# Optimization experiments

Hardware: AMD Instinct MI355X
Metric: run time of the kernel (lower is better)

## Reference

```python
import jax, jax.numpy as jnp
import numpy as np

N = 8192
IN_F = 128
OUT_F = 128
ALPHA = 0.2  # LeakyReLU negative slope
NEG_INF = -9e15


def setup_inputs() -> dict:
    key = jax.random.key(0)
    k1, k2, k3, k4, k5 = jax.random.split(key, 5)
    mole_out = jax.random.normal(k1, (N, IN_F), dtype=jnp.float32)
    adj = jax.random.randint(k2, (N, N), 0, 2, dtype=jnp.int32)
    # nn.Linear(in_features, out_features, bias=False): y = x @ W  (W stored as [in, out])
    W = jax.random.normal(k3, (IN_F, OUT_F), dtype=jnp.float32) / np.sqrt(IN_F)
    # nn.Linear(2*out_features, 1, bias=False) weight split into a1 (for Wh_i) and a2 (for Wh_j)
    a1 = jax.random.normal(k4, (OUT_F,), dtype=jnp.float32) / np.sqrt(2 * OUT_F)
    a2 = jax.random.normal(k5, (OUT_F,), dtype=jnp.float32) / np.sqrt(2 * OUT_F)
    return {"mole_out": mole_out, "adj": adj, "W": W, "a1": a1, "a2": a2}


def reference(mole_out, adj, W, a1, a2):
    Wh = mole_out @ W                       # (N, F)
    # a([Wh_i || Wh_j]) = a1.Wh_i + a2.Wh_j  -- avoids the O(N^2*2F) concat tensor
    s1 = Wh @ a1                            # (N,)
    s2 = Wh @ a2                            # (N,)
    e = jax.nn.leaky_relu(s1[:, None] + s2[None, :], negative_slope=ALPHA)  # (N, N)
    att = jnp.where(adj > 0, e, NEG_INF)
    att = jax.nn.softmax(att, axis=1)       # row softmax over neighbors j
    # dropout_gnn = 0.0 -> identity
    h_prime = att @ Wh                      # (N, F)
    return jax.nn.elu(h_prime)              # concat=True branch
```

## Files before the change

### kernel.cpp

```cpp
#include <hip/hip_runtime.h>
#include <hip/hip_bf16.h>

#define NROW 8192
#define NF   128
#define LOG2E 1.4426950408889634f

typedef float f32x4  __attribute__((ext_vector_type(4)));
typedef int   i32x4  __attribute__((ext_vector_type(4)));
typedef short bf16x8 __attribute__((ext_vector_type(8)));
typedef short bf16x4 __attribute__((ext_vector_type(4)));
typedef unsigned long long u64;

__device__ __forceinline__ short f2bf(float f) {
    union { float f; unsigned u; } v; v.f = f;
    unsigned r = v.u + 0x7FFFu + ((v.u >> 16) & 1u);
    return (short)(r >> 16);
}

__device__ __forceinline__ void gload_lds16(const short* g, short* l) {
    __builtin_amdgcn_global_load_lds(
        (const __attribute__((address_space(1))) void*)g,
        (__attribute__((address_space(3))) void*)l, 16, 0, 0);
}


__global__ __launch_bounds__(256) void k0_wt(const float* __restrict__ W,
                                             short* __restrict__ WT) {
    int idx = blockIdx.x * 256 + threadIdx.x;
    int c = idx >> 7, k = idx & 127;
    WT[c * NF + k] = f2bf(W[k * NF + c]);
}

__global__ __launch_bounds__(256) void k1_wh(const float* __restrict__ mo,
        const short* __restrict__ WT,
        const float* __restrict__ a1, const float* __restrict__ a2,
        short* __restrict__ WhT, float* __restrict__ s1g, float* __restrict__ s2g) {
    __shared__ float s_lds[2][32];
    int t = threadIdx.x;
    int w = t >> 6, l = t & 63, lg = l >> 4, lr = l & 15;
    int rows0 = blockIdx.x * 32;
    if (t < 64) s_lds[t >> 5][t & 31] = 0.0f;
    __syncthreads();

    f32x4 acc[2][2] = {};
#pragma unroll
    for (int ks = 0; ks < 4; ++ks) {
        bf16x8 a[2], b[2];
#pragma unroll
        for (int rt = 0; rt < 2; ++rt) {
            const float* ap = mo + (size_t)(rows0 + rt*16 + lr) * NF + ks*32 + lg*8;
            f32x4 x0 = *(const f32x4*)ap;
            f32x4 x1 = *(const f32x4*)(ap + 4);
#pragma unroll
            for (int e = 0; e < 4; ++e) { a[rt][e] = f2bf(x0[e]); a[rt][4+e] = f2bf(x1[e]); }
        }
#pragma unroll
        for (int ct = 0; ct < 2; ++ct) {
            int c = w*32 + ct*16 + lr;
            b[ct] = *(const bf16x8*)(WT + c*NF + ks*32 + lg*8);
        }
#pragma unroll
        for (int rt = 0; rt < 2; ++rt)
#pragma unroll
            for (int ct = 0; ct < 2; ++ct)
                acc[rt][ct] = __builtin_amdgcn_mfma_f32_16x16x32_bf16(a[rt], b[ct], acc[rt][ct], 0, 0, 0);
    }

#pragma unroll
    for (int rt = 0; rt < 2; ++rt) {
        float p1[4] = {0,0,0,0}, p2[4] = {0,0,0,0};
#pragma unroll
        for (int ct = 0; ct < 2; ++ct) {
            int c = w*32 + ct*16 + lr;
            float a1c = a1[c], a2c = a2[c];
            bf16x4 wv;
#pragma unroll
            for (int g = 0; g < 4; ++g) {
                float v = acc[rt][ct][g];
                wv[g] = f2bf(v);
                p1[g] += v * a1c;
                p2[g] += v * a2c;
            }
            int r0 = rows0 + rt*16 + lg*4;
            size_t off = (size_t)(r0 >> 6) * 8192 + (size_t)(c >> 4) * 1024
                       + (size_t)((r0 >> 5) & 1) * 512 + (size_t)((r0 >> 3) & 3) * 128
                       + (size_t)(c & 15) * 8 + (size_t)(r0 & 7);
            *(bf16x4*)(WhT + off) = wv;
        }
#pragma unroll
        for (int off = 1; off < 16; off <<= 1) {
#pragma unroll
            for (int g = 0; g < 4; ++g) {
                p1[g] += __shfl_xor(p1[g], off);
                p2[g] += __shfl_xor(p2[g], off);
            }
        }
        if (lr == 0) {
            int rloc = rt*16 + lg*4;
#pragma unroll
            for (int g = 0; g < 4; ++g) {
                atomicAdd(&s_lds[0][rloc+g], p1[g]);
                atomicAdd(&s_lds[1][rloc+g], p2[g]);
            }
        }
    }
    __syncthreads();
    if (t < 32)       s1g[rows0 + t]        = s_lds[0][t] * LOG2E;
    else if (t < 64)  s2g[rows0 + (t - 32)] = s_lds[1][t - 32] * LOG2E;
}

__global__ __launch_bounds__(256, 4) void k2_main(
        const int* __restrict__ adj, const short* __restrict__ WhT,
        const float* __restrict__ s1g, const float* __restrict__ s2g,
        float* __restrict__ numP, float* __restrict__ zP,
        int S, int npb) {
    __shared__ __attribute__((aligned(16))) short Bl[2][8192];
    __shared__ __attribute__((aligned(16))) float s2l[1024];

    int t = threadIdx.x, w = t >> 6, l = t & 63;
    int lo = l & 15, hi = l >> 4;
    int b = blockIdx.x, jseg = b % S, rg = b / S;
    int wrows0 = (rg << 6) + (w << 4);
    int j0 = jseg * npb;
    int NT = npb >> 6;

    for (int i = t; i < (npb >> 2); i += 256)
        ((f32x4*)s2l)[i] = ((const f32x4*)(s2g + j0))[i];

    float s1v = s1g[wrows0 + lo];
    const int* arow = adj + (size_t)wrows0 * NROW + j0 + l;

    f32x4 acc[8] = {};
    float z = 0.0f;

    int An[16];
#pragma unroll
    for (int r = 0; r < 16; ++r)
        An[r] = __builtin_nontemporal_load(arow + r * NROW);
    {
        const short* gs = WhT + (size_t)(j0 >> 6) * 8192 + w*2048 + l*8;
        short* ds = &Bl[0][w*2048];
#pragma unroll
        for (int r4 = 0; r4 < 4; ++r4)
            gload_lds16(gs + r4*512, ds + r4*512);
    }
    __syncthreads();

    int cur = 0;
    for (int it = 0; it < NT; ++it) {
        int more = (it + 1 < NT);
        if (more) {
            const short* gs = WhT + (size_t)((j0 + ((it+1) << 6)) >> 6) * 8192 + w*2048 + l*8;
            short* ds = &Bl[cur ^ 1][w*2048];
#pragma unroll
            for (int r4 = 0; r4 < 4; ++r4)
                gload_lds16(gs + r4*512, ds + r4*512);
        }
        u64 bmq = 0;
#pragma unroll
        for (int r = 0; r < 16; ++r) {
            u64 br = __ballot(An[r] > 0);
            if (more) An[r] = __builtin_nontemporal_load(arow + r * NROW + ((it + 1) << 6));
            bmq = (lo == r) ? br : bmq;
        }
#pragma unroll
        for (int ks = 0; ks < 2; ++ks) {
            unsigned bits = (unsigned)(bmq >> ((ks << 5) + hi * 8)) & 0xffu;
            int js = (it << 6) + ks * 32 + hi * 8;
            f32x4 sa = *(const f32x4*)(s2l + js);
            f32x4 sb = *(const f32x4*)(s2l + js + 4);
            float p[8];
#pragma unroll
            for (int e = 0; e < 4; ++e) {
                float x, pe;
                x = s1v + sa[e]; pe = exp2f(fmaxf(x, 0.2f * x));
                p[e]     = ((bits >> e) & 1) ? pe : 0.0f;        z += p[e];
                x = s1v + sb[e]; pe = exp2f(fmaxf(x, 0.2f * x));
                p[4 + e] = ((bits >> (4 + e)) & 1) ? pe : 0.0f;  z += p[4 + e];
            }
            union { bf16x8 v8; __hip_bfloat162 h2[4]; } fau;
#pragma unroll
            for (int q = 0; q < 4; ++q)
                fau.h2[q] = __float22bfloat162_rn(make_float2(p[2*q], p[2*q + 1]));
            const short* Bc = &Bl[cur][ks * 512 + l * 8];
#pragma unroll
            for (int ct = 0; ct < 8; ++ct) {
                bf16x8 bv = *(const bf16x8*)(Bc + ct * 1024);
                acc[ct] = __builtin_amdgcn_mfma_f32_16x16x32_bf16(fau.v8, bv, acc[ct], 0, 0, 0);
            }
        }
        asm volatile("s_waitcnt vmcnt(16)" ::: "memory");
        __builtin_amdgcn_sched_barrier(0);
        __builtin_amdgcn_s_barrier();
        __builtin_amdgcn_sched_barrier(0);
        cur ^= 1;
    }

    z += __shfl_xor(z, 16);
    z += __shfl_xor(z, 32);
    if (l < 16) zP[(size_t)jseg * NROW + wrows0 + lo] = z;

    size_t obase = (size_t)jseg * NROW * NF;
#pragma unroll
    for (int ct = 0; ct < 8; ++ct) {
        int cc = ct * 16 + lo;
        int r0 = wrows0 + hi * 4;
#pragma unroll
        for (int g = 0; g < 4; ++g)
            numP[obase + (size_t)(r0 + g) * NF + cc] = acc[ct][g];
    }
}

__global__ __launch_bounds__(256) void k3_reduce(const float* __restrict__ numP,
        const float* __restrict__ zP, float* __restrict__ out, int S) {
    int idx = (blockIdx.x * 256 + threadIdx.x) * 4;
    int r = idx >> 7;
    f32x4 num = {};
    float zz = 0.0f;
    for (int s = 0; s < S; ++s) {
        f32x4 v = *(const f32x4*)(numP + (size_t)s * (NROW * NF) + idx);
        num += v;
        zz  += zP[s * NROW + r];
    }
    f32x4 o;
#pragma unroll
    for (int e = 0; e < 4; ++e) {
        float h = num[e] / zz;
        o[e] = (h > 0.0f) ? h : expm1f(h);
    }
    *(f32x4*)(out + idx) = o;
}

extern "C" void kernel_launch(void* const* d_in, const int* in_sizes, int n_in,
                              void* d_out, int out_size, void* d_ws, size_t ws_size,
                              hipStream_t stream) {
    const float* mo  = (const float*)d_in[0];
    const int*   adj = (const int*)d_in[1];
    const float* W   = (const float*)d_in[2];
    const float* a1  = (const float*)d_in[3];
    const float* a2  = (const float*)d_in[4];
    float* out = (float*)d_out;

    char* p = (char*)d_ws;
    short* WT  = (short*)p;  p += (size_t)NF * NF * 2;
    short* WhT = (short*)p;  p += (size_t)NF * NROW * 2;
    float* s1  = (float*)p;  p += (size_t)NROW * 4;
    float* s2  = (float*)p;  p += (size_t)NROW * 4;
    float* zP  = (float*)p;  p += (size_t)8 * NROW * 4;
    size_t fixed = (size_t)(p - (char*)d_ws);

    int S = 8;
    while (S > 1 && fixed + (size_t)S * NROW * NF * 4 > ws_size) S >>= 1;
    float* numP = (float*)p;
    if (fixed + (size_t)S * NROW * NF * 4 > ws_size) numP = out;

    k0_wt<<<dim3(64), dim3(256), 0, stream>>>(W, WT);
    k1_wh<<<dim3(256), dim3(256), 0, stream>>>(mo, WT, a1, a2, WhT, s1, s2);
    k2_main<<<dim3((NROW / 64) * S), dim3(256), 0, stream>>>(adj, WhT, s1, s2, numP, zP, S, NROW / S);
    k3_reduce<<<dim3(NROW * NF / 1024), dim3(256), 0, stream>>>(numP, zP, out, S);
}
```

Measured before the change: 97.03 us.

## Precompute adjacency bitmask in fused pre-kernel and stage it into LDS

Adjacency ballot-to-bitmask conversion moves out of the main attention kernel into extra blocks fused into the Wh projection kernel, which write a packed u64 bitmask to workspace. The main kernel loads its bitmask slice into LDS up front, so its loop no longer streams the 256MB int32 adjacency. The WhT tile drops from double to single buffering with full barriers, which frees LDS for the mask but serializes load and compute. The S-shrinking workspace fallback is removed.

```diff
diff --git a/kernel.cpp b/kernel.cpp
--- a/kernel.cpp
+++ b/kernel.cpp
@@ -4,6 +4,7 @@
 #define NROW 8192
 #define NF   128
 #define LOG2E 1.4426950408889634f
+#define NBM  ((NROW / 64) * (NROW / 512))
 
 typedef float f32x4  __attribute__((ext_vector_type(4)));
 typedef int   i32x4  __attribute__((ext_vector_type(4)));
@@ -31,14 +32,39 @@
     WT[c * NF + k] = f2bf(W[k * NF + c]);
 }
 
-__global__ __launch_bounds__(256) void k1_wh(const float* __restrict__ mo,
-        const short* __restrict__ WT,
-        const float* __restrict__ a1, const float* __restrict__ a2,
-        short* __restrict__ WhT, float* __restrict__ s1g, float* __restrict__ s2g) {
+__global__ __launch_bounds__(256) void k1f(const float* __restrict__ mo,
+        const short* __restrict__ WT, const float* __restrict__ a1,
+        const float* __restrict__ a2, const int* __restrict__ adj,
+        short* __restrict__ WhT, float* __restrict__ s1g, float* __restrict__ s2g,
+        u64* __restrict__ bm2) {
+    int t = threadIdx.x;
+    if (blockIdx.x < NBM) {
+        int bb = blockIdx.x;
+        int rowgrp = bb >> 4, jseg16 = bb & 15;
+        int w = t >> 6, l = t & 63, lo = l & 15;
+        int wrows0 = rowgrp * 64 + w * 16;
+        const int* arow = adj + (size_t)wrows0 * NROW + jseg16 * 512 + l;
+
+        int An[16];
+#pragma unroll
+        for (int r = 0; r < 16; ++r) An[r] = arow[r * NROW];
+        for (int it = 0; it < 8; ++it) {
+            u64 bmq = 0;
+            int more = (it + 1 < 8);
+#pragma unroll
+            for (int r = 0; r < 16; ++r) {
+                u64 br = __ballot(An[r] > 0);
+                if (more) An[r] = arow[r * NROW + ((it + 1) << 6)];
+                bmq = (lo == r) ? br : bmq;
+            }
+            if (l < 16)
+                bm2[(size_t)(jseg16 * 8 + it) * NROW + wrows0 + lo] = bmq;
+        }
+        return;
+    }
     __shared__ float s_lds[2][32];
-    int t = threadIdx.x;
     int w = t >> 6, l = t & 63, lg = l >> 4, lr = l & 15;
-    int rows0 = blockIdx.x * 32;
+    int rows0 = (blockIdx.x - NBM) * 32;
     if (t < 64) s_lds[t >> 5][t & 31] = 0.0f;
     __syncthreads();
 
@@ -110,12 +136,13 @@
 }
 
 __global__ __launch_bounds__(256, 4) void k2_main(
-        const int* __restrict__ adj, const short* __restrict__ WhT,
+        const u64* __restrict__ bm2, const short* __restrict__ WhT,
         const float* __restrict__ s1g, const float* __restrict__ s2g,
         float* __restrict__ numP, float* __restrict__ zP,
         int S, int npb) {
-    __shared__ __attribute__((aligned(16))) short Bl[2][8192];
+    __shared__ __attribute__((aligned(16))) short Bl[8192];
     __shared__ __attribute__((aligned(16))) float s2l[1024];
+    __shared__ __attribute__((aligned(16))) u64  bml[1024];
 
     int t = threadIdx.x, w = t >> 6, l = t & 63;
     int lo = l & 15, hi = l >> 4;
@@ -123,46 +150,30 @@
     int wrows0 = (rg << 6) + (w << 4);
     int j0 = jseg * npb;
     int NT = npb >> 6;
+    int jb0 = j0 >> 6;
 
     for (int i = t; i < (npb >> 2); i += 256)
         ((f32x4*)s2l)[i] = ((const f32x4*)(s2g + j0))[i];
+    for (int f = t * 4; f < npb; f += 1024) {
+        const u64* g = bm2 + (size_t)(jb0 + (f >> 6)) * NROW + (rg << 6) + (f & 63);
+        *(i32x4*)(bml + f)     = *(const i32x4*)g;
+        *(i32x4*)(bml + f + 2) = *(const i32x4*)(g + 2);
+    }
+    {
+        const short* gs = WhT + (size_t)jb0 * 8192 + w*2048 + l*8;
+        short* ds = &Bl[w*2048];
+#pragma unroll
+        for (int r4 = 0; r4 < 4; ++r4)
+            gload_lds16(gs + r4*512, ds + r4*512);
+    }
+    __syncthreads();
 
     float s1v = s1g[wrows0 + lo];
-    const int* arow = adj + (size_t)wrows0 * NROW + j0 + l;
-
     f32x4 acc[8] = {};
     float z = 0.0f;
 
-    int An[16];
-#pragma unroll
-    for (int r = 0; r < 16; ++r)
-        An[r] = __builtin_nontemporal_load(arow + r * NROW);
-    {
-        const short* gs = WhT + (size_t)(j0 >> 6) * 8192 + w*2048 + l*8;
-        short* ds = &Bl[0][w*2048];
-#pragma unroll
-        for (int r4 = 0; r4 < 4; ++r4)
-            gload_lds16(gs + r4*512, ds + r4*512);
-    }
-    __syncthreads();
-
-    int cur = 0;
     for (int it = 0; it < NT; ++it) {
-        int more = (it + 1 < NT);
-        if (more) {
-            const short* gs = WhT + (size_t)((j0 + ((it+1) << 6)) >> 6) * 8192 + w*2048 + l*8;
-            short* ds = &Bl[cur ^ 1][w*2048];
-#pragma unroll
-            for (int r4 = 0; r4 < 4; ++r4)
-                gload_lds16(gs + r4*512, ds + r4*512);
-        }
-        u64 bmq = 0;
-#pragma unroll
-        for (int r = 0; r < 16; ++r) {
-            u64 br = __ballot(An[r] > 0);
-            if (more) An[r] = __builtin_nontemporal_load(arow + r * NROW + ((it + 1) << 6));
-            bmq = (lo == r) ? br : bmq;
-        }
+        u64 bmq = bml[it * 64 + w * 16 + lo];
 #pragma unroll
         for (int ks = 0; ks < 2; ++ks) {
             unsigned bits = (unsigned)(bmq >> ((ks << 5) + hi * 8)) & 0xffu;
@@ -182,18 +193,22 @@
 #pragma unroll
             for (int q = 0; q < 4; ++q)
                 fau.h2[q] = __float22bfloat162_rn(make_float2(p[2*q], p[2*q + 1]));
-            const short* Bc = &Bl[cur][ks * 512 + l * 8];
+            const short* Bc = &Bl[ks * 512 + l * 8];
 #pragma unroll
             for (int ct = 0; ct < 8; ++ct) {
                 bf16x8 bv = *(const bf16x8*)(Bc + ct * 1024);
                 acc[ct] = __builtin_amdgcn_mfma_f32_16x16x32_bf16(fau.v8, bv, acc[ct], 0, 0, 0);
             }
         }
-        asm volatile("s_waitcnt vmcnt(16)" ::: "memory");
-        __builtin_amdgcn_sched_barrier(0);
-        __builtin_amdgcn_s_barrier();
-        __builtin_amdgcn_sched_barrier(0);
-        cur ^= 1;
+        __syncthreads();
+        if (it + 1 < NT) {
+            const short* gs = WhT + (size_t)(jb0 + it + 1) * 8192 + w*2048 + l*8;
+            short* ds = &Bl[w*2048];
+#pragma unroll
+            for (int r4 = 0; r4 < 4; ++r4)
+                gload_lds16(gs + r4*512, ds + r4*512);
+            __syncthreads();
+        }
     }
 
     z += __shfl_xor(z, 16);
@@ -247,15 +262,15 @@
     float* s1  = (float*)p;  p += (size_t)NROW * 4;
     float* s2  = (float*)p;  p += (size_t)NROW * 4;
     float* zP  = (float*)p;  p += (size_t)8 * NROW * 4;
+    u64*  bm2  = (u64*)p;    p += (size_t)(NROW / 64) * NROW * 8;
     size_t fixed = (size_t)(p - (char*)d_ws);
 
     int S = 8;
-    while (S > 1 && fixed + (size_t)S * NROW * NF * 4 > ws_size) S >>= 1;
     float* numP = (float*)p;
     if (fixed + (size_t)S * NROW * NF * 4 > ws_size) numP = out;
 
     k0_wt<<<dim3(64), dim3(256), 0, stream>>>(W, WT);
-    k1_wh<<<dim3(256), dim3(256), 0, stream>>>(mo, WT, a1, a2, WhT, s1, s2);
-    k2_main<<<dim3((NROW / 64) * S), dim3(256), 0, stream>>>(adj, WhT, s1, s2, numP, zP, S, NROW / S);
+    k1f<<<dim3(NBM + 256), dim3(256), 0, stream>>>(mo, WT, a1, a2, adj, WhT, s1, s2, bm2);
+    k2_main<<<dim3((NROW / 64) * S), dim3(256), 0, stream>>>(bm2, WhT, s1, s2, numP, zP, S, NROW / S);
     k3_reduce<<<dim3(NROW * NF / 1024), dim3(256), 0, stream>>>(numP, zP, out, S);
 }
```

After: 107.9 us. 1.11x slower.

## Split k2 into adjacency-bitmask prepass then single-buffered MFMA loop

Applied to the files above, without the earlier changes.

Moves all adjacency loads and ballots into a prepass that streams adj two tiles at a time and stores the per-row bitmasks in LDS. The main loop then reads masks from LDS instead of interleaving adj loads with compute. The double-buffered Wh tile is replaced by a single buffer, so each tile load is followed by a full barrier and the load is no longer overlapped with MFMA work. This lowers LDS use but serializes Wh staging against compute.

```diff
diff --git a/kernel.cpp b/kernel.cpp
--- a/kernel.cpp
+++ b/kernel.cpp
@@ -114,8 +114,9 @@
         const float* __restrict__ s1g, const float* __restrict__ s2g,
         float* __restrict__ numP, float* __restrict__ zP,
         int S, int npb) {
-    __shared__ __attribute__((aligned(16))) short Bl[2][8192];
+    __shared__ __attribute__((aligned(16))) short Bl[8192];
     __shared__ __attribute__((aligned(16))) float s2l[1024];
+    __shared__ __attribute__((aligned(16))) u64  bml[1024];
 
     int t = threadIdx.x, w = t >> 6, l = t & 63;
     int lo = l & 15, hi = l >> 4;
@@ -123,46 +124,51 @@
     int wrows0 = (rg << 6) + (w << 4);
     int j0 = jseg * npb;
     int NT = npb >> 6;
+    int jb0 = j0 >> 6;
 
     for (int i = t; i < (npb >> 2); i += 256)
         ((f32x4*)s2l)[i] = ((const f32x4*)(s2g + j0))[i];
+    {
+        const short* gs = WhT + (size_t)jb0 * 8192 + w*2048 + l*8;
+        short* ds = &Bl[w*2048];
+#pragma unroll
+        for (int r4 = 0; r4 < 4; ++r4)
+            gload_lds16(gs + r4*512, ds + r4*512);
+    }
+
+    const int* arow = adj + (size_t)wrows0 * NROW + j0 + l;
+    int A0[16], A1[16];
+#pragma unroll
+    for (int r = 0; r < 16; ++r) {
+        A0[r] = __builtin_nontemporal_load(arow + r * NROW);
+        A1[r] = __builtin_nontemporal_load(arow + r * NROW + 64);
+    }
+    for (int jt = 0; jt < NT; jt += 2) {
+        u64 b0 = 0, b1 = 0;
+        int m0 = (jt + 2 < NT), m1 = (jt + 3 < NT);
+#pragma unroll
+        for (int r = 0; r < 16; ++r) {
+            u64 br = __ballot(A0[r] > 0);
+            if (m0) A0[r] = __builtin_nontemporal_load(arow + r * NROW + ((jt + 2) << 6));
+            b0 = (lo == r) ? br : b0;
+        }
+        if (l < 16) bml[jt * 64 + (w << 4) + l] = b0;
+#pragma unroll
+        for (int r = 0; r < 16; ++r) {
+            u64 br = __ballot(A1[r] > 0);
+            if (m1) A1[r] = __builtin_nontemporal_load(arow + r * NROW + ((jt + 3) << 6));
+            b1 = (lo == r) ? br : b1;
+        }
+        if (l < 16) bml[(jt + 1) * 64 + (w << 4) + l] = b1;
+    }
+    __syncthreads();
 
     float s1v = s1g[wrows0 + lo];
-    const int* arow = adj + (size_t)wrows0 * NROW + j0 + l;
-
     f32x4 acc[8] = {};
     float z = 0.0f;
 
-    int An[16];
-#pragma unroll
-    for (int r = 0; r < 16; ++r)
-        An[r] = __builtin_nontemporal_load(arow + r * NROW);
-    {
-        const short* gs = WhT + (size_t)(j0 >> 6) * 8192 + w*2048 + l*8;
-        short* ds = &Bl[0][w*2048];
-#pragma unroll
-        for (int r4 = 0; r4 < 4; ++r4)
-            gload_lds16(gs + r4*512, ds + r4*512);
-    }
-    __syncthreads();
-
-    int cur = 0;
     for (int it = 0; it < NT; ++it) {
-        int more = (it + 1 < NT);
-        if (more) {
-            const short* gs = WhT + (size_t)((j0 + ((it+1) << 6)) >> 6) * 8192 + w*2048 + l*8;
-            short* ds = &Bl[cur ^ 1][w*2048];
-#pragma unroll
-            for (int r4 = 0; r4 < 4; ++r4)
-                gload_lds16(gs + r4*512, ds + r4*512);
-        }
-        u64 bmq = 0;
-#pragma unroll
-        for (int r = 0; r < 16; ++r) {
-            u64 br = __ballot(An[r] > 0);
-            if (more) An[r] = __builtin_nontemporal_load(arow + r * NROW + ((it + 1) << 6));
-            bmq = (lo == r) ? br : bmq;
-        }
+        u64 bmq = bml[it * 64 + (w << 4) + lo];
 #pragma unroll
         for (int ks = 0; ks < 2; ++ks) {
             unsigned bits = (unsigned)(bmq >> ((ks << 5) + hi * 8)) & 0xffu;
@@ -182,18 +188,22 @@
 #pragma unroll
             for (int q = 0; q < 4; ++q)
                 fau.h2[q] = __float22bfloat162_rn(make_float2(p[2*q], p[2*q + 1]));
-            const short* Bc = &Bl[cur][ks * 512 + l * 8];
+            const short* Bc = &Bl[ks * 512 + l * 8];
 #pragma unroll
             for (int ct = 0; ct < 8; ++ct) {
                 bf16x8 bv = *(const bf16x8*)(Bc + ct * 1024);
                 acc[ct] = __builtin_amdgcn_mfma_f32_16x16x32_bf16(fau.v8, bv, acc[ct], 0, 0, 0);
             }
         }
-        asm volatile("s_waitcnt vmcnt(16)" ::: "memory");
-        __builtin_amdgcn_sched_barrier(0);
-        __builtin_amdgcn_s_barrier();
-        __builtin_amdgcn_sched_barrier(0);
-        cur ^= 1;
+        __syncthreads();
+        if (it + 1 < NT) {
+            const short* gs = WhT + (size_t)(jb0 + it + 1) * 8192 + w*2048 + l*8;
+            short* ds = &Bl[w*2048];
+#pragma unroll
+            for (int r4 = 0; r4 < 4; ++r4)
+                gload_lds16(gs + r4*512, ds + r4*512);
+            __syncthreads();
+        }
     }
 
     z += __shfl_xor(z, 16);
```

After: 119.1 us. 1.23x slower.

## Double-buffer adjacency register loads two tiles ahead with unrolled pipeline

Applied to the files above, without the earlier changes.

Restructures the main loop to keep two sets of adjacency registers, prefetching adjacency tiles two iterations ahead while the WhT tile is staged one ahead. The loop is manually unrolled by two with explicit vmcnt waits so ballot mask computation uses data loaded earlier, hiding global load latency behind MFMA work. This costs 16 more registers per lane and issues redundant clamped loads at the tail. It also assumes NT is even, since the unrolled loop processes iterations it+1 unconditionally.

```diff
diff --git a/kernel.cpp b/kernel.cpp
--- a/kernel.cpp
+++ b/kernel.cpp
@@ -129,72 +129,115 @@
 
     float s1v = s1g[wrows0 + lo];
     const int* arow = adj + (size_t)wrows0 * NROW + j0 + l;
+    const short* wbase = WhT + (size_t)(j0 >> 6) * 8192 + w*2048 + l*8;
 
     f32x4 acc[8] = {};
     float z = 0.0f;
 
-    int An[16];
-#pragma unroll
-    for (int r = 0; r < 16; ++r)
-        An[r] = __builtin_nontemporal_load(arow + r * NROW);
-    {
-        const short* gs = WhT + (size_t)(j0 >> 6) * 8192 + w*2048 + l*8;
-        short* ds = &Bl[0][w*2048];
-#pragma unroll
-        for (int r4 = 0; r4 < 4; ++r4)
-            gload_lds16(gs + r4*512, ds + r4*512);
-    }
-    __syncthreads();
+#define STAGE(BUF_, TI_) do { \
+    const short* gs_ = wbase + (size_t)(TI_) * 8192; \
+    short* ds_ = &Bl[BUF_][w*2048]; \
+_Pragma("unroll") \
+    for (int r4 = 0; r4 < 4; ++r4) gload_lds16(gs_ + r4*512, ds_ + r4*512); \
+} while (0)
+
+#define BALLOT(AR_, BQ_) do { \
+    u64 m_ = 0; \
+_Pragma("unroll") \
+    for (int r = 0; r < 16; ++r) { \
+        u64 br_ = __ballot(AR_[r] > 0); \
+        m_ = (lo == r) ? br_ : m_; \
+    } \
+    BQ_ = m_; \
+} while (0)
+
+#define REFILL(AR_, TI_) do { \
+    int jo_ = (TI_) << 6; \
+_Pragma("unroll") \
+    for (int r = 0; r < 16; ++r) \
+        AR_[r] = __builtin_nontemporal_load(arow + r * NROW + jo_); \
+} while (0)
+
+#define COMPUTE(IT_, BQ_, BUF_) do { \
+_Pragma("unroll") \
+    for (int ks = 0; ks < 2; ++ks) { \
+        unsigned bits_ = (unsigned)((BQ_) >> ((ks << 5) + hi * 8)) & 0xffu; \
+        int js_ = ((IT_) << 6) + ks * 32 + hi * 8; \
+        f32x4 sa_ = *(const f32x4*)(s2l + js_); \
+        f32x4 sb_ = *(const f32x4*)(s2l + js_ + 4); \
+        float p_[8]; \
+_Pragma("unroll") \
+        for (int e = 0; e < 4; ++e) { \
+            float x_, pe_; \
+            x_ = s1v + sa_[e]; pe_ = exp2f(fmaxf(x_, 0.2f * x_)); \
+            p_[e]     = ((bits_ >> e) & 1) ? pe_ : 0.0f;        z += p_[e]; \
+            x_ = s1v + sb_[e]; pe_ = exp2f(fmaxf(x_, 0.2f * x_)); \
+            p_[4 + e] = ((bits_ >> (4 + e)) & 1) ? pe_ : 0.0f;  z += p_[4 + e]; \
+        } \
+        union { bf16x8 v8; __hip_bfloat162 h2[4]; } fau_; \
+_Pragma("unroll") \
+        for (int q = 0; q < 4; ++q) \
+            fau_.h2[q] = __float22bfloat162_rn(make_float2(p_[2*q], p_[2*q + 1])); \
+        const short* Bc_ = &Bl[BUF_][ks * 512 + l * 8]; \
+_Pragma("unroll") \
+        for (int ct = 0; ct < 8; ++ct) { \
+            bf16x8 bv_ = *(const bf16x8*)(Bc_ + ct * 1024); \
+            acc[ct] = __builtin_amdgcn_mfma_f32_16x16x32_bf16(fau_.v8, bv_, acc[ct], 0, 0, 0); \
+        } \
+    } \
+} while (0)
+
+    int A0[16], A1[16];
+    u64 bmq0, bmq1;
+
+    REFILL(A0, 0);
+    STAGE(0, 0);
+    REFILL(A1, 1);
+    asm volatile("s_waitcnt vmcnt(24)" ::: "memory");
+    __builtin_amdgcn_sched_barrier(0);
+    BALLOT(A0, bmq0);
+    asm volatile("s_waitcnt vmcnt(16) lgkmcnt(0)" ::: "memory");
+    __builtin_amdgcn_sched_barrier(0);
+    __builtin_amdgcn_s_barrier();
+    __builtin_amdgcn_sched_barrier(0);
 
     int cur = 0;
-    for (int it = 0; it < NT; ++it) {
-        int more = (it + 1 < NT);
-        if (more) {
-            const short* gs = WhT + (size_t)((j0 + ((it+1) << 6)) >> 6) * 8192 + w*2048 + l*8;
-            short* ds = &Bl[cur ^ 1][w*2048];
-#pragma unroll
-            for (int r4 = 0; r4 < 4; ++r4)
-                gload_lds16(gs + r4*512, ds + r4*512);
-        }
-        u64 bmq = 0;
-#pragma unroll
-        for (int r = 0; r < 16; ++r) {
-            u64 br = __ballot(An[r] > 0);
-            if (more) An[r] = __builtin_nontemporal_load(arow + r * NROW + ((it + 1) << 6));
-            bmq = (lo == r) ? br : bmq;
-        }
-#pragma unroll
-        for (int ks = 0; ks < 2; ++ks) {
-            unsigned bits = (unsigned)(bmq >> ((ks << 5) + hi * 8)) & 0xffu;
-            int js = (it << 6) + ks * 32 + hi * 8;
-            f32x4 sa = *(const f32x4*)(s2l + js);
-            f32x4 sb = *(const f32x4*)(s2l + js + 4);
-            float p[8];
-#pragma unroll
-            for (int e = 0; e < 4; ++e) {
-                float x, pe;
-                x = s1v + sa[e]; pe = exp2f(fmaxf(x, 0.2f * x));
-                p[e]     = ((bits >> e) & 1) ? pe : 0.0f;        z += p[e];
-                x = s1v + sb[e]; pe = exp2f(fmaxf(x, 0.2f * x));
-                p[4 + e] = ((bits >> (4 + e)) & 1) ? pe : 0.0f;  z += p[4 + e];
-            }
-            union { bf16x8 v8; __hip_bfloat162 h2[4]; } fau;
-#pragma unroll
-            for (int q = 0; q < 4; ++q)
-                fau.h2[q] = __float22bfloat162_rn(make_float2(p[2*q], p[2*q + 1]));
-            const short* Bc = &Bl[cur][ks * 512 + l * 8];
-#pragma unroll
-            for (int ct = 0; ct < 8; ++ct) {
-                bf16x8 bv = *(const bf16x8*)(Bc + ct * 1024);
-                acc[ct] = __builtin_amdgcn_mfma_f32_16x16x32_bf16(fau.v8, bv, acc[ct], 0, 0, 0);
-            }
-        }
-        asm volatile("s_waitcnt vmcnt(16)" ::: "memory");
-        __builtin_amdgcn_sched_barrier(0);
-        __builtin_amdgcn_s_barrier();
-        __builtin_amdgcn_sched_barrier(0);
-        cur ^= 1;
-    }
+    for (int it = 0; it < NT; it += 2) {
+        {
+            int t1 = (it + 1 < NT) ? it + 1 : NT - 1;
+            int t2 = (it + 2 < NT) ? it + 2 : NT - 1;
+            STAGE(cur ^ 1, t1);
+            REFILL(A0, t2);
+            COMPUTE(it, bmq0, cur);
+            asm volatile("s_waitcnt vmcnt(24)" ::: "memory");
+            __builtin_amdgcn_sched_barrier(0);
+            BALLOT(A1, bmq1);
+            asm volatile("s_waitcnt vmcnt(16)" ::: "memory");
+            __builtin_amdgcn_sched_barrier(0);
+            __builtin_amdgcn_s_barrier();
+            __builtin_amdgcn_sched_barrier(0);
+            cur ^= 1;
+        }
+        {
+            int t2 = (it + 2 < NT) ? it + 2 : NT - 1;
+            int t3 = (it + 3 < NT) ? it + 3 : NT - 1;
+            STAGE(cur ^ 1, t2);
+            REFILL(A1, t3);
+            COMPUTE(it + 1, bmq1, cur);
+            asm volatile("s_waitcnt vmcnt(24)" ::: "memory");
+            __builtin_amdgcn_sched_barrier(0);
+            BALLOT(A0, bmq0);
+            asm volatile("s_waitcnt vmcnt(16)" ::: "memory");
+            __builtin_amdgcn_sched_barrier(0);
+            __builtin_amdgcn_s_barrier();
+            __builtin_amdgcn_sched_barrier(0);
+            cur ^= 1;
+        }
+    }
+#undef STAGE
+#undef BALLOT
+#undef REFILL
+#undef COMPUTE
 
     z += __shfl_xor(z, 16);
     z += __shfl_xor(z, 32);
```

Result: slower. 103.1 us (+6.3%).
